# Kernel tuning notes

Hardware: AMD Instinct MI355X
Metric: run time of the kernel (lower is better)

Reference implementation:

```python
import jax, jax.numpy as jnp
import numpy as np

N_NODES = 8192
HIDDEN = 256
HEADS = 4
HEAD_DIM = HIDDEN // HEADS
NUM_EDGES = 4096
NUM_INC = 65536
LN_EPS = 1e-5


def setup_inputs() -> dict:
    key = jax.random.key(0)
    ks = jax.random.split(key, 8)
    scale = HIDDEN ** -0.5
    return {
        "x": jax.random.normal(ks[0], (N_NODES, HIDDEN), jnp.float32),
        "node_idx": jax.random.randint(ks[1], (NUM_INC,), 0, N_NODES),
        "edge_idx": jax.random.randint(ks[2], (NUM_INC,), 0, NUM_EDGES),
        "W_w": jax.random.normal(ks[3], (HIDDEN, HIDDEN), jnp.float32) * scale,
        "W_b": jax.random.normal(ks[4], (HIDDEN,), jnp.float32) * 0.02,
        "edge_att": jax.random.normal(ks[5], (HEADS, HEAD_DIM), jnp.float32) * scale,
        "out_w": jax.random.normal(ks[6], (HIDDEN, HIDDEN), jnp.float32) * scale,
        "out_b": jax.random.normal(ks[7], (HIDDEN,), jnp.float32) * 0.02,
    }


def reference(x, node_idx, edge_idx, W_w, W_b, edge_att, out_w, out_b):
    n = x.shape[0]
    e = node_idx.shape[0]
    # x' = W(x), split into heads: [N, heads, head_dim]
    xw = (x @ W_w.T + W_b).reshape(n, HEADS, HEAD_DIM)
    feat = xw[node_idx]                                   # [E, heads, hd]
    logits = jnp.einsum("ehd,hd->eh", feat, edge_att)      # [E, heads]
    # segment softmax over nodes within each hyperedge, per head
    seg_max = jax.ops.segment_max(logits, edge_idx, num_segments=NUM_EDGES)
    p = jnp.exp(logits - seg_max[edge_idx])
    seg_sum = jax.ops.segment_sum(p, edge_idx, num_segments=NUM_EDGES)
    attn = p / seg_sum[edge_idx]                           # [E, heads]
    attn_mean = attn.mean(axis=1)                          # mean over heads, [E]
    # hyperedges with < 2 nodes are skipped in the original
    sizes = jax.ops.segment_sum(jnp.ones((e,), x.dtype), edge_idx, num_segments=NUM_EDGES)
    valid = sizes[edge_idx] >= 2.0
    attn_mean = jnp.where(valid, attn_mean, 0.0)
    # scatter-add attention-weighted ORIGINAL features back to nodes
    contrib = attn_mean[:, None] * x[node_idx]             # [E, H]
    out = jnp.zeros_like(x).at[node_idx].add(contrib)
    # degree normalization counts ALL incidences (including size-1 edges)
    counts = jnp.zeros((n,), x.dtype).at[node_idx].add(1.0)
    out = out / jnp.clip(counts, 1.0)[:, None]
    out = out @ out_w.T + out_b
    # fresh nn.LayerNorm => affine identity, biased variance, eps=1e-5
    mu = out.mean(-1, keepdims=True)
    var = ((out - mu) ** 2).mean(-1, keepdims=True)
    out = (out - mu) / jnp.sqrt(var + LN_EPS)
    # NxN pairwise attention accumulation: AW[i,j] = sum_e attn_i(e)*count_j(e), diag zeroed
    A = jnp.zeros((n, NUM_EDGES), x.dtype).at[node_idx, edge_idx].add(attn_mean)
    B = jnp.zeros((n, NUM_EDGES), x.dtype).at[node_idx, edge_idx].add(1.0)
    attention_weights = A @ B.T
    attention_weights = attention_weights.at[jnp.diag_indices(n)].set(0.0)
    return out, attention_weights
```

## Files before the change

kernel.cpp:

```cpp
#include <hip/hip_runtime.h>
#include <stdint.h>

#define N_NODES  8192
#define HIDDEN   256
#define HEADS    4
#define HEAD_DIM 64
#define NUM_EDGES 4096
#define NUM_INC  65536
#define LN_EPS   1e-5f

typedef unsigned int uint_t;


#define OFF_SEGSUM   0
#define OFF_SEGSIZE  65536
#define OFF_NODECNT  81920
#define OFF_NODEFILL 114688
#define OFF_EDGEFILL 147456
#define OFF_WNODE    163840
#define ZERO_BYTES   196608
#define OFF_VKH      196608
#define OFF_BL       200704
#define OFF_LOGIT    200960
#define OFF_NODEPTR  332032
#define OFF_EDGEPTR  365056
#define OFF_NODEINC  381696
#define OFF_EDGEMEM  643840
#define OFF_ATTN     905984

__global__ __launch_bounds__(256) void k_zero(uint_t* __restrict__ w) {
    w[blockIdx.x * 256 + threadIdx.x] = 0u;
}

__global__ __launch_bounds__(256) void k_fold(const float* __restrict__ Ww,
                                              const float* __restrict__ Wb,
                                              const float* __restrict__ ea,
                                              float* __restrict__ vkh,
                                              float* __restrict__ bl) {
    int k = threadIdx.x, h = blockIdx.x;
    float a = 0.f;
    for (int d = 0; d < HEAD_DIM; ++d)
        a += ea[h * HEAD_DIM + d] * Ww[(size_t)(h * HEAD_DIM + d) * HIDDEN + k];
    vkh[k * HEADS + h] = a;
    if (k == 0) {
        float b = 0.f;
        for (int d = 0; d < HEAD_DIM; ++d)
            b += Wb[h * HEAD_DIM + d] * ea[h * HEAD_DIM + d];
        bl[h] = b;
    }
}

__global__ __launch_bounds__(256) void k_logits(const float* __restrict__ x,
                                                const float* __restrict__ vkh,
                                                const float* __restrict__ bl,
                                                float* __restrict__ logit) {
    __shared__ float vs[HIDDEN * HEADS];
    __shared__ float bls[HEADS];
    int t = threadIdx.x;
    for (int j = t; j < HIDDEN * HEADS; j += 256) vs[j] = vkh[j];
    if (t < HEADS) bls[t] = bl[t];
    __syncthreads();
    int n = blockIdx.x * 64 + (t >> 2);
    int h = t & 3;
    const float* xr = x + (size_t)n * HIDDEN;
    float acc = bls[h];
    for (int k = 0; k < HIDDEN; ++k)
        acc += xr[k] * vs[k * HEADS + h];
    logit[n * HEADS + h] = acc;
}

__global__ void k_pass1(const int* __restrict__ node_idx, const int* __restrict__ edge_idx,
                        const float* __restrict__ logit, float* __restrict__ seg_sum,
                        int* __restrict__ seg_size, int* __restrict__ node_cnt) {
    int i = blockIdx.x * 256 + threadIdx.x;
    int n = node_idx[i], e = edge_idx[i];
    #pragma unroll
    for (int h = 0; h < HEADS; ++h)
        atomicAdd(&seg_sum[e * HEADS + h], __expf(logit[n * HEADS + h]));
    atomicAdd(&seg_size[e], 1);
    atomicAdd(&node_cnt[n], 1);
}

__global__ __launch_bounds__(256) void k_scan(const int* __restrict__ node_cnt, int* __restrict__ node_ptr,
                                              const int* __restrict__ seg_size, int* __restrict__ edge_ptr) {
    __shared__ int part[256];
    const int* cnt; int* ptr; int n;
    if (blockIdx.x == 0) { cnt = node_cnt; ptr = node_ptr; n = N_NODES; }
    else                 { cnt = seg_size; ptr = edge_ptr; n = NUM_EDGES; }
    int t = threadIdx.x, C = n / 256;
    int s = 0;
    for (int j = 0; j < C; ++j) s += cnt[t * C + j];
    part[t] = s;
    __syncthreads();
    if (t == 0) {
        int run = 0;
        for (int i = 0; i < 256; ++i) { int tmp = part[i]; part[i] = run; run += tmp; }
        ptr[n] = run;
    }
    __syncthreads();
    int run = part[t];
    for (int j = 0; j < C; ++j) { ptr[t * C + j] = run; run += cnt[t * C + j]; }
}

__global__ void k_fill(const int* __restrict__ node_idx, const int* __restrict__ edge_idx,
                       const int* __restrict__ node_ptr, const int* __restrict__ edge_ptr,
                       int* __restrict__ node_fill, int* __restrict__ edge_fill,
                       int* __restrict__ node_inc, int* __restrict__ edge_mem) {
    int i = blockIdx.x * 256 + threadIdx.x;
    int n = node_idx[i], e = edge_idx[i];
    int p = node_ptr[n] + atomicAdd(&node_fill[n], 1);
    node_inc[p] = i;
    int q = edge_ptr[e] + atomicAdd(&edge_fill[e], 1);
    edge_mem[q] = n;
}

__global__ void k_attn(const int* __restrict__ node_idx, const int* __restrict__ edge_idx,
                       const float* __restrict__ logit, const float* __restrict__ seg_sum,
                       const int* __restrict__ seg_size, float* __restrict__ attn,
                       float* __restrict__ w_node) {
    int i = blockIdx.x * 256 + threadIdx.x;
    int e = edge_idx[i];
    float a = 0.f;
    if (seg_size[e] >= 2) {
        int n = node_idx[i];
        float s = 0.f;
        #pragma unroll
        for (int h = 0; h < HEADS; ++h)
            s += __expf(logit[n * HEADS + h]) / seg_sum[e * HEADS + h];
        a = 0.25f * s;
        atomicAdd(&w_node[n], a);
    }
    attn[i] = a;
}

__global__ __launch_bounds__(256) void k_out(const float* __restrict__ x,
                                             const float* __restrict__ w_node,
                                             const int* __restrict__ node_cnt,
                                             const float* __restrict__ out_w,
                                             const float* __restrict__ out_b,
                                             float* __restrict__ out) {
    __shared__ float y[16][HIDDEN + 1];
    __shared__ float sr[16], mu_s[16], rs_s[16];
    int t = threadIdx.x;
    int R = blockIdx.x * 16;
    if (t < 16) {
        int n = R + t;
        int c = node_cnt[n]; if (c < 1) c = 1;
        sr[t] = w_node[n] / (float)c;
    }
    __syncthreads();
    #pragma unroll
    for (int r = 0; r < 16; ++r)
        y[r][t] = sr[r] * x[(size_t)(R + r) * HIDDEN + t];
    __syncthreads();
    float acc[16];
    float bias = out_b[t];
    #pragma unroll
    for (int r = 0; r < 16; ++r) acc[r] = bias;
    const float* wr = out_w + (size_t)t * HIDDEN;
    for (int j = 0; j < HIDDEN; ++j) {
        float w = wr[j];
        #pragma unroll
        for (int r = 0; r < 16; ++r) acc[r] += y[r][j] * w;
    }
    __syncthreads();
    #pragma unroll
    for (int r = 0; r < 16; ++r) y[r][t] = acc[r];
    __syncthreads();
    if (t < 16) {
        float m = 0.f;
        for (int j = 0; j < HIDDEN; ++j) m += y[t][j];
        m *= (1.0f / HIDDEN);
        float s2 = 0.f;
        for (int j = 0; j < HIDDEN; ++j) { float d = y[t][j] - m; s2 += d * d; }
        mu_s[t] = m;
        rs_s[t] = rsqrtf(s2 * (1.0f / HIDDEN) + LN_EPS);
    }
    __syncthreads();
    #pragma unroll
    for (int r = 0; r < 16; ++r)
        out[(size_t)(R + r) * HIDDEN + t] = (y[r][t] - mu_s[r]) * rs_s[r];
}

__global__ __launch_bounds__(256) void k_aw(const float* __restrict__ attn,
                                            const int* __restrict__ node_ptr,
                                            const int* __restrict__ node_inc,
                                            const int* __restrict__ edge_ptr,
                                            const int* __restrict__ edge_mem,
                                            const int* __restrict__ edge_idx,
                                            float* __restrict__ AW) {
    __shared__ __align__(16) float row[N_NODES];
    int t = threadIdx.x;
    int i = blockIdx.x;
    for (int c = t; c < N_NODES; c += 256) row[c] = 0.f;
    __syncthreads();
    int pb = node_ptr[i], pe = node_ptr[i + 1];
    for (int p = pb; p < pe; ++p) {
        int m = node_inc[p];
        float a = attn[m];
        if (a != 0.f) {
            int e = edge_idx[m];
            int qb = edge_ptr[e], qe = edge_ptr[e + 1];
            for (int q = qb + t; q < qe; q += 256)
                atomicAdd(&row[edge_mem[q]], a);
        }
    }
    __syncthreads();
    if (t == 0) row[i] = 0.f;
    __syncthreads();
    float4* dst = (float4*)(AW + (size_t)i * N_NODES);
    const float4* src = (const float4*)row;
    for (int c = t; c < N_NODES / 4; c += 256)
        dst[c] = src[c];
}

extern "C" void kernel_launch(void* const* d_in, const int* in_sizes, int n_in,
                              void* d_out, int out_size, void* d_ws, size_t ws_size,
                              hipStream_t stream) {
    const float* x        = (const float*)d_in[0];
    const int*   node_idx = (const int*)d_in[1];
    const int*   edge_idx = (const int*)d_in[2];
    const float* Ww       = (const float*)d_in[3];
    const float* Wb       = (const float*)d_in[4];
    const float* ea       = (const float*)d_in[5];
    const float* ow       = (const float*)d_in[6];
    const float* ob       = (const float*)d_in[7];
    float* out0 = (float*)d_out;
    float* aw   = out0 + (size_t)N_NODES * HIDDEN;

    char* ws = (char*)d_ws;
    float* seg_sum   = (float*)(ws + OFF_SEGSUM);
    int*   seg_size  = (int*)(ws + OFF_SEGSIZE);
    int*   node_cnt  = (int*)(ws + OFF_NODECNT);
    int*   node_fill = (int*)(ws + OFF_NODEFILL);
    int*   edge_fill = (int*)(ws + OFF_EDGEFILL);
    float* w_node    = (float*)(ws + OFF_WNODE);
    float* vkh       = (float*)(ws + OFF_VKH);
    float* bl        = (float*)(ws + OFF_BL);
    float* logit     = (float*)(ws + OFF_LOGIT);
    int*   node_ptr  = (int*)(ws + OFF_NODEPTR);
    int*   edge_ptr  = (int*)(ws + OFF_EDGEPTR);
    int*   node_inc  = (int*)(ws + OFF_NODEINC);
    int*   edge_mem  = (int*)(ws + OFF_EDGEMEM);
    float* attn      = (float*)(ws + OFF_ATTN);

    k_zero<<<ZERO_BYTES / 4 / 256, 256, 0, stream>>>((uint_t*)ws);
    k_fold<<<HEADS, 256, 0, stream>>>(Ww, Wb, ea, vkh, bl);
    k_logits<<<N_NODES / 64, 256, 0, stream>>>(x, vkh, bl, logit);
    k_pass1<<<NUM_INC / 256, 256, 0, stream>>>(node_idx, edge_idx, logit, seg_sum, seg_size, node_cnt);
    k_scan<<<2, 256, 0, stream>>>(node_cnt, node_ptr, seg_size, edge_ptr);
    k_fill<<<NUM_INC / 256, 256, 0, stream>>>(node_idx, edge_idx, node_ptr, edge_ptr,
                                              node_fill, edge_fill, node_inc, edge_mem);
    k_attn<<<NUM_INC / 256, 256, 0, stream>>>(node_idx, edge_idx, logit, seg_sum, seg_size, attn, w_node);
    k_out<<<N_NODES / 16, 256, 0, stream>>>(x, w_node, node_cnt, ow, ob, out0);
    k_aw<<<N_NODES, 256, 0, stream>>>(attn, node_ptr, node_inc, edge_ptr, edge_mem, edge_idx, aw);
}
```

Before: 436.3 us.

## Replace float atomics with CSR gathers and vectorize logits, out GEMM, AW rows

Segment exp-sums and per-node attention weights are now computed by gathering over the CSR lists (new k_seg kernel, and a loop inside k_out) instead of float atomicAdd scatter. k_logits stages x rows into shared memory with float4 loads and uses a transposed folded weight. k_out reads out_w and y as float4. k_aw splits incidences across four wavefronts, each looping over its edge's members with 64 lanes instead of 256 threads. This removes global float atomic contention and improves load vectorization, at the cost of one extra launch and serial per-thread loops for large segments.

```diff
diff --git a/kernel.cpp b/kernel.cpp
--- a/kernel.cpp
+++ b/kernel.cpp
@@ -12,21 +12,20 @@
 typedef unsigned int uint_t;
 
 
-#define OFF_SEGSUM   0
-#define OFF_SEGSIZE  65536
-#define OFF_NODECNT  81920
-#define OFF_NODEFILL 114688
-#define OFF_EDGEFILL 147456
-#define OFF_WNODE    163840
-#define ZERO_BYTES   196608
-#define OFF_VKH      196608
-#define OFF_BL       200704
-#define OFF_LOGIT    200960
-#define OFF_NODEPTR  332032
-#define OFF_EDGEPTR  365056
-#define OFF_NODEINC  381696
-#define OFF_EDGEMEM  643840
-#define OFF_ATTN     905984
+#define OFF_SEGSZ    0
+#define OFF_NCNT     16384
+#define OFF_NFILL    49152
+#define OFF_EFILL    81920
+#define ZERO_BYTES   98304
+#define OFF_VKH      98304
+#define OFF_BL       102400
+#define OFF_LOGIT    102464
+#define OFF_NPTR     233536
+#define OFF_EPTR     266320
+#define OFF_SEGSUM   282720
+#define OFF_NINC     348256
+#define OFF_EMEM     610400
+#define OFF_ATTN     872544
 
 __global__ __launch_bounds__(256) void k_zero(uint_t* __restrict__ w) {
     w[blockIdx.x * 256 + threadIdx.x] = 0u;
@@ -35,13 +34,13 @@
 __global__ __launch_bounds__(256) void k_fold(const float* __restrict__ Ww,
                                               const float* __restrict__ Wb,
                                               const float* __restrict__ ea,
-                                              float* __restrict__ vkh,
+                                              float* __restrict__ vkhT,
                                               float* __restrict__ bl) {
     int k = threadIdx.x, h = blockIdx.x;
     float a = 0.f;
     for (int d = 0; d < HEAD_DIM; ++d)
         a += ea[h * HEAD_DIM + d] * Ww[(size_t)(h * HEAD_DIM + d) * HIDDEN + k];
-    vkh[k * HEADS + h] = a;
+    vkhT[h * HIDDEN + k] = a;
     if (k == 0) {
         float b = 0.f;
         for (int d = 0; d < HEAD_DIM; ++d)
@@ -51,34 +50,38 @@
 }
 
 __global__ __launch_bounds__(256) void k_logits(const float* __restrict__ x,
-                                                const float* __restrict__ vkh,
+                                                const float* __restrict__ vkhT,
                                                 const float* __restrict__ bl,
                                                 float* __restrict__ logit) {
-    __shared__ float vs[HIDDEN * HEADS];
+    __shared__ __align__(16) float xs[32 * HIDDEN];
+    __shared__ __align__(16) float vs[HEADS * HIDDEN];
     __shared__ float bls[HEADS];
-    int t = threadIdx.x;
-    for (int j = t; j < HIDDEN * HEADS; j += 256) vs[j] = vkh[j];
+    int t = threadIdx.x, b = blockIdx.x;
+    float4* xsv = (float4*)xs;
+    const float4* xg = (const float4*)(x + (size_t)b * 32 * HIDDEN);
+    #pragma unroll
+    for (int i = 0; i < 8; ++i) xsv[i * 256 + t] = xg[i * 256 + t];
+    ((float4*)vs)[t] = ((const float4*)vkhT)[t];
     if (t < HEADS) bls[t] = bl[t];
     __syncthreads();
-    int n = blockIdx.x * 64 + (t >> 2);
-    int h = t & 3;
-    const float* xr = x + (size_t)n * HIDDEN;
-    float acc = bls[h];
-    for (int k = 0; k < HIDDEN; ++k)
-        acc += xr[k] * vs[k * HEADS + h];
-    logit[n * HEADS + h] = acc;
+    if (t < 128) {
+        int n = t >> 2, h = t & 3;
+        const float4* xr = (const float4*)(xs + n * HIDDEN);
+        const float4* vr = (const float4*)(vs + h * HIDDEN);
+        float acc = bls[h];
+        for (int k4 = 0; k4 < HIDDEN / 4; ++k4) {
+            float4 xv = xr[k4], vv = vr[k4];
+            acc += xv.x * vv.x + xv.y * vv.y + xv.z * vv.z + xv.w * vv.w;
+        }
+        logit[(b * 32 + n) * HEADS + h] = acc;
+    }
 }
 
 __global__ void k_pass1(const int* __restrict__ node_idx, const int* __restrict__ edge_idx,
-                        const float* __restrict__ logit, float* __restrict__ seg_sum,
                         int* __restrict__ seg_size, int* __restrict__ node_cnt) {
     int i = blockIdx.x * 256 + threadIdx.x;
-    int n = node_idx[i], e = edge_idx[i];
-    #pragma unroll
-    for (int h = 0; h < HEADS; ++h)
-        atomicAdd(&seg_sum[e * HEADS + h], __expf(logit[n * HEADS + h]));
-    atomicAdd(&seg_size[e], 1);
-    atomicAdd(&node_cnt[n], 1);
+    atomicAdd(&seg_size[edge_idx[i]], 1);
+    atomicAdd(&node_cnt[node_idx[i]], 1);
 }
 
 __global__ __launch_bounds__(256) void k_scan(const int* __restrict__ node_cnt, int* __restrict__ node_ptr,
@@ -114,10 +117,27 @@
     edge_mem[q] = n;
 }
 
+__global__ __launch_bounds__(256) void k_seg(const int* __restrict__ edge_ptr,
+                                             const int* __restrict__ edge_mem,
+                                             const float* __restrict__ logit,
+                                             float* __restrict__ seg_sum) {
+    int e = blockIdx.x * 256 + threadIdx.x;
+    int qb = edge_ptr[e], qe = edge_ptr[e + 1];
+    float s0 = 0, s1 = 0, s2 = 0, s3 = 0;
+    for (int q = qb; q < qe; ++q) {
+        int j = edge_mem[q];
+        s0 += __expf(logit[j * 4 + 0]);
+        s1 += __expf(logit[j * 4 + 1]);
+        s2 += __expf(logit[j * 4 + 2]);
+        s3 += __expf(logit[j * 4 + 3]);
+    }
+    seg_sum[e * 4 + 0] = s0; seg_sum[e * 4 + 1] = s1;
+    seg_sum[e * 4 + 2] = s2; seg_sum[e * 4 + 3] = s3;
+}
+
 __global__ void k_attn(const int* __restrict__ node_idx, const int* __restrict__ edge_idx,
                        const float* __restrict__ logit, const float* __restrict__ seg_sum,
-                       const int* __restrict__ seg_size, float* __restrict__ attn,
-                       float* __restrict__ w_node) {
+                       const int* __restrict__ seg_size, float* __restrict__ attn) {
     int i = blockIdx.x * 256 + threadIdx.x;
     int e = edge_idx[i];
     float a = 0.f;
@@ -128,25 +148,28 @@
         for (int h = 0; h < HEADS; ++h)
             s += __expf(logit[n * HEADS + h]) / seg_sum[e * HEADS + h];
         a = 0.25f * s;
-        atomicAdd(&w_node[n], a);
     }
     attn[i] = a;
 }
 
 __global__ __launch_bounds__(256) void k_out(const float* __restrict__ x,
-                                             const float* __restrict__ w_node,
-                                             const int* __restrict__ node_cnt,
+                                             const int* __restrict__ node_ptr,
+                                             const int* __restrict__ node_inc,
+                                             const float* __restrict__ attn,
                                              const float* __restrict__ out_w,
                                              const float* __restrict__ out_b,
                                              float* __restrict__ out) {
-    __shared__ float y[16][HIDDEN + 1];
+    __shared__ __align__(16) float y[16][260];
     __shared__ float sr[16], mu_s[16], rs_s[16];
     int t = threadIdx.x;
     int R = blockIdx.x * 16;
     if (t < 16) {
         int n = R + t;
-        int c = node_cnt[n]; if (c < 1) c = 1;
-        sr[t] = w_node[n] / (float)c;
+        int pb = node_ptr[n], pe = node_ptr[n + 1];
+        float w = 0.f;
+        for (int p = pb; p < pe; ++p) w += attn[node_inc[p]];
+        int c = pe - pb; if (c < 1) c = 1;
+        sr[t] = w / (float)c;
     }
     __syncthreads();
     #pragma unroll
@@ -157,11 +180,14 @@
     float bias = out_b[t];
     #pragma unroll
     for (int r = 0; r < 16; ++r) acc[r] = bias;
-    const float* wr = out_w + (size_t)t * HIDDEN;
-    for (int j = 0; j < HIDDEN; ++j) {
-        float w = wr[j];
+    const float4* wr4 = (const float4*)(out_w + (size_t)t * HIDDEN);
+    for (int j4 = 0; j4 < HIDDEN / 4; ++j4) {
+        float4 wv = wr4[j4];
         #pragma unroll
-        for (int r = 0; r < 16; ++r) acc[r] += y[r][j] * w;
+        for (int r = 0; r < 16; ++r) {
+            float4 yv = *(const float4*)&y[r][j4 * 4];
+            acc[r] += yv.x * wv.x + yv.y * wv.y + yv.z * wv.z + yv.w * wv.w;
+        }
     }
     __syncthreads();
     #pragma unroll
@@ -190,18 +216,20 @@
                                             const int* __restrict__ edge_idx,
                                             float* __restrict__ AW) {
     __shared__ __align__(16) float row[N_NODES];
-    int t = threadIdx.x;
+    int t = threadIdx.x, w = t >> 6, lane = t & 63;
     int i = blockIdx.x;
-    for (int c = t; c < N_NODES; c += 256) row[c] = 0.f;
+    float4* rowv = (float4*)row;
+    #pragma unroll
+    for (int c = 0; c < 8; ++c) rowv[c * 256 + t] = make_float4(0.f, 0.f, 0.f, 0.f);
     __syncthreads();
     int pb = node_ptr[i], pe = node_ptr[i + 1];
-    for (int p = pb; p < pe; ++p) {
+    for (int p = pb + w; p < pe; p += 4) {
         int m = node_inc[p];
         float a = attn[m];
         if (a != 0.f) {
             int e = edge_idx[m];
             int qb = edge_ptr[e], qe = edge_ptr[e + 1];
-            for (int q = qb + t; q < qe; q += 256)
+            for (int q = qb + lane; q < qe; q += 64)
                 atomicAdd(&row[edge_mem[q]], a);
         }
     }
@@ -209,9 +237,8 @@
     if (t == 0) row[i] = 0.f;
     __syncthreads();
     float4* dst = (float4*)(AW + (size_t)i * N_NODES);
-    const float4* src = (const float4*)row;
-    for (int c = t; c < N_NODES / 4; c += 256)
-        dst[c] = src[c];
+    #pragma unroll
+    for (int c = 0; c < 8; ++c) dst[c * 256 + t] = rowv[c * 256 + t];
 }
 
 extern "C" void kernel_launch(void* const* d_in, const int* in_sizes, int n_in,
@@ -229,29 +256,29 @@
     float* aw   = out0 + (size_t)N_NODES * HIDDEN;
 
     char* ws = (char*)d_ws;
-    float* seg_sum   = (float*)(ws + OFF_SEGSUM);
-    int*   seg_size  = (int*)(ws + OFF_SEGSIZE);
-    int*   node_cnt  = (int*)(ws + OFF_NODECNT);
-    int*   node_fill = (int*)(ws + OFF_NODEFILL);
-    int*   edge_fill = (int*)(ws + OFF_EDGEFILL);
-    float* w_node    = (float*)(ws + OFF_WNODE);
-    float* vkh       = (float*)(ws + OFF_VKH);
+    int*   seg_size  = (int*)(ws + OFF_SEGSZ);
+    int*   node_cnt  = (int*)(ws + OFF_NCNT);
+    int*   node_fill = (int*)(ws + OFF_NFILL);
+    int*   edge_fill = (int*)(ws + OFF_EFILL);
+    float* vkhT      = (float*)(ws + OFF_VKH);
     float* bl        = (float*)(ws + OFF_BL);
     float* logit     = (float*)(ws + OFF_LOGIT);
-    int*   node_ptr  = (int*)(ws + OFF_NODEPTR);
-    int*   edge_ptr  = (int*)(ws + OFF_EDGEPTR);
-    int*   node_inc  = (int*)(ws + OFF_NODEINC);
-    int*   edge_mem  = (int*)(ws + OFF_EDGEMEM);
+    int*   node_ptr  = (int*)(ws + OFF_NPTR);
+    int*   edge_ptr  = (int*)(ws + OFF_EPTR);
+    float* seg_sum   = (float*)(ws + OFF_SEGSUM);
+    int*   node_inc  = (int*)(ws + OFF_NINC);
+    int*   edge_mem  = (int*)(ws + OFF_EMEM);
     float* attn      = (float*)(ws + OFF_ATTN);
 
     k_zero<<<ZERO_BYTES / 4 / 256, 256, 0, stream>>>((uint_t*)ws);
-    k_fold<<<HEADS, 256, 0, stream>>>(Ww, Wb, ea, vkh, bl);
-    k_logits<<<N_NODES / 64, 256, 0, stream>>>(x, vkh, bl, logit);
-    k_pass1<<<NUM_INC / 256, 256, 0, stream>>>(node_idx, edge_idx, logit, seg_sum, seg_size, node_cnt);
+    k_fold<<<HEADS, 256, 0, stream>>>(Ww, Wb, ea, vkhT, bl);
+    k_logits<<<N_NODES / 32, 256, 0, stream>>>(x, vkhT, bl, logit);
+    k_pass1<<<NUM_INC / 256, 256, 0, stream>>>(node_idx, edge_idx, seg_size, node_cnt);
     k_scan<<<2, 256, 0, stream>>>(node_cnt, node_ptr, seg_size, edge_ptr);
     k_fill<<<NUM_INC / 256, 256, 0, stream>>>(node_idx, edge_idx, node_ptr, edge_ptr,
                                               node_fill, edge_fill, node_inc, edge_mem);
-    k_attn<<<NUM_INC / 256, 256, 0, stream>>>(node_idx, edge_idx, logit, seg_sum, seg_size, attn, w_node);
-    k_out<<<N_NODES / 16, 256, 0, stream>>>(x, w_node, node_cnt, ow, ob, out0);
+    k_seg<<<NUM_EDGES / 256, 256, 0, stream>>>(edge_ptr, edge_mem, logit, seg_sum);
+    k_attn<<<NUM_INC / 256, 256, 0, stream>>>(node_idx, edge_idx, logit, seg_sum, seg_size, attn);
+    k_out<<<N_NODES / 16, 256, 0, stream>>>(x, node_ptr, node_inc, attn, ow, ob, out0);
     k_aw<<<N_NODES, 256, 0, stream>>>(attn, node_ptr, node_inc, edge_ptr, edge_mem, edge_idx, aw);
 }
```

New measurement: 398.2 us. 1.1x faster.
